# Kernel tuning notes

Measured on AMD Instinct MI355X. Metric: run time of the kernel, lower is better.

The kernel has to match this reference:

```python
import jax, jax.numpy as jnp
import numpy as np

N_NODES = 40000
N_EDGES = 640000
D_IN = 128
D_OUT = 128
ALPHA = 0.5   # real-valued complex alpha from init
Q = 0.25      # magnetic potential parameter


def setup_inputs() -> dict:
    key = jax.random.key(0)
    k = jax.random.split(key, 6)
    x = jax.random.normal(k[0], (N_NODES, D_IN), dtype=jnp.float32)
    edge_index = jax.random.randint(k[1], (2, N_EDGES), 0, N_NODES, dtype=jnp.int32)
    W1 = jax.random.normal(k[2], (D_IN, D_OUT), dtype=jnp.float32) * 0.05
    b1 = jax.random.normal(k[3], (D_OUT,), dtype=jnp.float32) * 0.05
    W2 = jax.random.normal(k[4], (D_IN, D_OUT), dtype=jnp.float32) * 0.05
    b2 = jax.random.normal(k[5], (D_OUT,), dtype=jnp.float32) * 0.05
    return {"x": x, "edge_index": edge_index, "W1": W1, "b1": b1, "W2": W2, "b2": b2}


def _magnet_spmm(x, edge_index, q):
    """y = H @ x where H = D_s^{-1/2} (A_s * exp(i*2*pi*q*(A - A^T))) D_s^{-1/2},
    A_s = 0.5*(A + A^T). Returns (y_real, y_imag); x is real (zero imag part)."""
    n = x.shape[0]
    row, col = edge_index[0], edge_index[1]
    e = row.shape[0]
    # detect whether the reverse edge (col,row) exists in the edge set
    keys = row * n + col
    rkeys = col * n + row
    sk = jnp.sort(keys)
    pos = jnp.searchsorted(sk, rkeys)
    has_rev = (pos < e) & (sk[jnp.clip(pos, 0, e - 1)] == rkeys)
    # symmetrize: each directed edge contributes 0.5 in both directions.
    # forward copy carries phase sign +1, reversed copy sign -1; phase is 0
    # when both directions exist (A - A^T = 0 there).
    r_all = jnp.concatenate([row, col])          # [2E]
    c_all = jnp.concatenate([col, row])
    sign = jnp.concatenate([jnp.ones((e,), x.dtype), -jnp.ones((e,), x.dtype)])
    hr = jnp.concatenate([has_rev, has_rev]).astype(x.dtype)
    theta = (2.0 * np.pi * q) * sign * (1.0 - hr)
    half = jnp.asarray(0.5, x.dtype)
    # symmetrized degree: deg[u] = sum_v A_s[u,v]
    deg = jax.ops.segment_sum(jnp.full((2 * e,), 0.5, x.dtype), r_all, num_segments=n)
    dinv = jnp.where(deg > 0, 1.0 / jnp.sqrt(deg), 0.0)
    scale = half * dinv[r_all] * dinv[c_all]
    val_re = scale * jnp.cos(theta)
    val_im = scale * jnp.sin(theta)
    xg = x[c_all]                                # [2E, D] gather
    y_re = jax.ops.segment_sum(val_re[:, None] * xg, r_all, num_segments=n)
    y_im = jax.ops.segment_sum(val_im[:, None] * xg, r_all, num_segments=n)
    return y_re, y_im


def reference(x, edge_index, W1, b1, W2, b2):
    y_re, y_im = _magnet_spmm(x, edge_index, Q)
    # alpha * lin1(y) + (1-alpha) * lin2(y), applied to real and imag parts
    out_re = ALPHA * (y_re @ W1 + b1) + (1.0 - ALPHA) * (y_re @ W2 + b2)
    out_im = ALPHA * (y_im @ W1 + b1) + (1.0 - ALPHA) * (y_im @ W2 + b2)
    return jnp.concatenate([out_re, out_im], axis=1)  # [N, 2*D_OUT]
```

## Files before the change

### kernel.cpp

```cpp
#include <hip/hip_runtime.h>
#include <math.h>

#define N_NODES 40000
#define D 128
#define NEDGE 640000
#define CAP 80

__device__ __forceinline__ unsigned short bf16rn(float f) {
    unsigned u = __float_as_uint(f);
    unsigned r = u + 0x7FFFu + ((u >> 16) & 1u);
    return (unsigned short)(r >> 16);
}

__global__ void init_kernel(int* __restrict__ cursorA, int* __restrict__ cursorB,
                            const float* __restrict__ W1, const float* __restrict__ b1,
                            const float* __restrict__ W2, const float* __restrict__ b2,
                            float* __restrict__ Wc, float* __restrict__ bc) {
    int i = blockIdx.x * blockDim.x + threadIdx.x;
    int stride = gridDim.x * blockDim.x;
    for (int t = i; t < N_NODES; t += stride) { cursorA[t] = 0; cursorB[t] = 0; }
    for (int t = i; t < D * D; t += stride) Wc[t] = 0.5f * (W1[t] + W2[t]);
    if (i < D) bc[i] = 0.5f * (b1[i] + b2[i]);
}

__global__ void expand_kernel(const int* __restrict__ row, const int* __restrict__ col,
                              int* __restrict__ cursorA, int* __restrict__ cursorB,
                              unsigned short* __restrict__ entries,
                              const float* __restrict__ x, unsigned short* __restrict__ xb) {
    int i = blockIdx.x * blockDim.x + threadIdx.x;
    int gstride = gridDim.x * blockDim.x;
    for (int e = i; e < NEDGE; e += gstride) {
        int r = row[e], c = col[e];
        int p1 = atomicAdd(&cursorA[r], 1);
        if (p1 < CAP) entries[(size_t)r * CAP + p1] = (unsigned short)c;
        int p2 = atomicAdd(&cursorB[c], 1);
        if (p2 < CAP) entries[(size_t)c * CAP + (CAP - 1 - p2)] = (unsigned short)r;
    }
    if (xb) {
        for (int t = i; t < N_NODES * D / 4; t += gstride) {
            float4 v = ((const float4*)x)[t];
            ushort4 o;
            o.x = bf16rn(v.x); o.y = bf16rn(v.y); o.z = bf16rn(v.z); o.w = bf16rn(v.w);
            ((ushort4*)xb)[t] = o;
        }
    }
}

template <int USE_BF16>
__global__ __launch_bounds__(256) void fused_kernel(
    const float* __restrict__ x, const unsigned short* __restrict__ xb,
    const unsigned short* __restrict__ entries,
    const int* __restrict__ cursorA, const int* __restrict__ cursorB,
    const float* __restrict__ Wc, const float* __restrict__ bc,
    float* __restrict__ out) {
    __shared__ unsigned short rawlds[4][2][CAP];
    __shared__ uint2 slds[4][2][CAP];
    __shared__ float ylds[8][260];

    int tid = threadIdx.x;
    int wave = tid >> 6, half = (tid >> 5) & 1, l = tid & 31;
    int n = wave * 2 + half;
    int u = blockIdx.x * 8 + n;

    int cA = cursorA[u], cB = cursorB[u];
    int a = min(cA, CAP);
    int b = min(cB, CAP - a);
    int m = a + b;
    int cnt = cA + cB;
    float dinv_u = (cnt > 0) ? rsqrtf(0.5f * (float)cnt) : 0.f;
    const unsigned short* eb = entries + (size_t)u * CAP;
    int gap = CAP - m;

    for (int t = l; t < m; t += 32)
        rawlds[wave][half][t] = eb[t < a ? t : t + gap];
    __builtin_amdgcn_wave_barrier();

    for (int t = l; t < m; t += 32) {
        unsigned short src = rawlds[wave][half][t];
        bool d1 = (t >= a);
        int lo = d1 ? 0 : a, hi = d1 ? a : m;
        bool rev = false;
        for (int j = lo; j < hi; ++j)
            rev |= (rawlds[wave][half][j] == src);
        int cs = cursorA[src] + cursorB[src];
        float s = 0.5f * dinv_u * rsqrtf(0.5f * (float)max(cs, 1));
        unsigned flag = 0u;
        float sval;
        if (rev) { sval = s; flag = 0x10000u; }
        else     { sval = d1 ? -s : s; }
        slds[wave][half][t] = make_uint2((unsigned)src | flag, __float_as_uint(sval));
    }
    __builtin_amdgcn_wave_barrier();

    float4 accre = make_float4(0.f, 0.f, 0.f, 0.f);
    float4 accim = make_float4(0.f, 0.f, 0.f, 0.f);

    if (USE_BF16) {
        #pragma unroll 8
        for (int i = 0; i < m; ++i) {
            uint2 t = slds[wave][half][i];
            unsigned src = t.x & 0xFFFFu;
            float s = __uint_as_float(t.y);
            bool isre = (t.x & 0x10000u) != 0u;
            float fre = isre ? s : 0.f;
            float fim = isre ? 0.f : s;
            uint2 v = ((const uint2*)(xb + (size_t)src * D))[l];
            float v0 = __uint_as_float(v.x << 16);
            float v1 = __uint_as_float(v.x & 0xFFFF0000u);
            float v2 = __uint_as_float(v.y << 16);
            float v3 = __uint_as_float(v.y & 0xFFFF0000u);
            accre.x += fre * v0; accre.y += fre * v1;
            accre.z += fre * v2; accre.w += fre * v3;
            accim.x += fim * v0; accim.y += fim * v1;
            accim.z += fim * v2; accim.w += fim * v3;
        }
    } else {
        #pragma unroll 4
        for (int i = 0; i < m; ++i) {
            uint2 t = slds[wave][half][i];
            unsigned src = t.x & 0xFFFFu;
            float s = __uint_as_float(t.y);
            bool isre = (t.x & 0x10000u) != 0u;
            float fre = isre ? s : 0.f;
            float fim = isre ? 0.f : s;
            float4 v = ((const float4*)(x + (size_t)src * D))[l];
            accre.x += fre * v.x; accre.y += fre * v.y;
            accre.z += fre * v.z; accre.w += fre * v.w;
            accim.x += fim * v.x; accim.y += fim * v.y;
            accim.z += fim * v.z; accim.w += fim * v.w;
        }
    }

    *(float4*)&ylds[n][l * 4] = accre;
    *(float4*)&ylds[n][128 + l * 4] = accim;
    __syncthreads();

    int n2 = tid >> 5, c = tid & 31;
    int u2 = blockIdx.x * 8 + n2;
    const float* yb = &ylds[n2][0];
    const float4* Wc4 = (const float4*)Wc;
    float4 ar = make_float4(0.f, 0.f, 0.f, 0.f);
    float4 ai = make_float4(0.f, 0.f, 0.f, 0.f);
    #pragma unroll 4
    for (int k = 0; k < 128; k += 4) {
        float4 yr4 = *(const float4*)&yb[k];
        float4 yi4 = *(const float4*)&yb[128 + k];
        #pragma unroll
        for (int j = 0; j < 4; ++j) {
            float4 w = Wc4[(k + j) * 32 + c];
            float yr = (j == 0) ? yr4.x : (j == 1) ? yr4.y : (j == 2) ? yr4.z : yr4.w;
            float yi = (j == 0) ? yi4.x : (j == 1) ? yi4.y : (j == 2) ? yi4.z : yi4.w;
            ar.x += yr * w.x; ar.y += yr * w.y; ar.z += yr * w.z; ar.w += yr * w.w;
            ai.x += yi * w.x; ai.y += yi * w.y; ai.z += yi * w.z; ai.w += yi * w.w;
        }
    }
    float4 bv = ((const float4*)bc)[c];
    ar.x += bv.x; ar.y += bv.y; ar.z += bv.z; ar.w += bv.w;
    ai.x += bv.x; ai.y += bv.y; ai.z += bv.z; ai.w += bv.w;
    *(float4*)&out[(size_t)u2 * 256 + c * 4] = ar;
    *(float4*)&out[(size_t)u2 * 256 + 128 + c * 4] = ai;
}

extern "C" void kernel_launch(void* const* d_in, const int* in_sizes, int n_in,
                              void* d_out, int out_size, void* d_ws, size_t ws_size,
                              hipStream_t stream) {
    const float* x  = (const float*)d_in[0];
    const int*   ei = (const int*)d_in[1];
    const float* W1 = (const float*)d_in[2];
    const float* b1 = (const float*)d_in[3];
    const float* W2 = (const float*)d_in[4];
    const float* b2 = (const float*)d_in[5];
    float* out = (float*)d_out;
    const int* row = ei;
    const int* col = ei + NEDGE;

    char* ws = (char*)d_ws;
    float*          Wc      = (float*)ws;
    float*          bc      = (float*)(ws + 65536);
    int*            cursorA = (int*)(ws + 66048);
    int*            cursorB = (int*)(ws + 226048);
    unsigned short* entries = (unsigned short*)(ws + 386048);
    const size_t xoff = 6786048;
    const size_t XBB = (size_t)N_NODES * D * 2;

    unsigned short* xb = nullptr;
    bool bf16 = false;
    if (ws_size >= xoff + XBB) {
        xb = (unsigned short*)(ws + xoff);
        bf16 = true;
    }

    init_kernel<<<512, 256, 0, stream>>>(cursorA, cursorB, W1, b1, W2, b2, Wc, bc);
    expand_kernel<<<2500, 256, 0, stream>>>(row, col, cursorA, cursorB, entries, x, xb);
    if (bf16) {
        fused_kernel<1><<<N_NODES / 8, 256, 0, stream>>>(x, xb, entries, cursorA, cursorB,
                                                         Wc, bc, out);
    } else {
        fused_kernel<0><<<N_NODES / 8, 256, 0, stream>>>(x, xb, entries, cursorA, cursorB,
                                                         Wc, bc, out);
    }
}
```

Measured before the change: 196.3 us.

## Apply combined linear layer before sparse aggregation and gather bf16 projected features

Uses linearity to reorder the computation as (H x) W = H (x W). A new dense GEMM kernel computes z = x·0.5(W1+W2) into bf16, also zeroing the cursors. The gather kernel then aggregates z directly and adds the bias, so the per-node dense projection after aggregation and its LDS staging are removed. The per-node matmul previously ran on both the real and imaginary parts, so the dense work is halved. The cost is a separate GEMM pass with an extra bf16 write and read of z, plus bf16 rounding applied after the projection instead of to x. The fp32 fallback path is dropped and a larger workspace is assumed.

```diff
diff --git a/kernel.cpp b/kernel.cpp
--- a/kernel.cpp
+++ b/kernel.cpp
@@ -5,6 +5,7 @@
 #define D 128
 #define NEDGE 640000
 #define CAP 80
+#define ZNB 64
 
 __device__ __forceinline__ unsigned short bf16rn(float f) {
     unsigned u = __float_as_uint(f);
@@ -12,21 +13,63 @@
     return (unsigned short)(r >> 16);
 }
 
-__global__ void init_kernel(int* __restrict__ cursorA, int* __restrict__ cursorB,
-                            const float* __restrict__ W1, const float* __restrict__ b1,
-                            const float* __restrict__ W2, const float* __restrict__ b2,
-                            float* __restrict__ Wc, float* __restrict__ bc) {
-    int i = blockIdx.x * blockDim.x + threadIdx.x;
-    int stride = gridDim.x * blockDim.x;
-    for (int t = i; t < N_NODES; t += stride) { cursorA[t] = 0; cursorB[t] = 0; }
-    for (int t = i; t < D * D; t += stride) Wc[t] = 0.5f * (W1[t] + W2[t]);
-    if (i < D) bc[i] = 0.5f * (b1[i] + b2[i]);
+__global__ __launch_bounds__(256) void zgemm_kernel(
+    const float* __restrict__ x, const float* __restrict__ W1, const float* __restrict__ W2,
+    unsigned short* __restrict__ z, int* __restrict__ cursorA, int* __restrict__ cursorB) {
+    int tid = threadIdx.x;
+    int gtid = blockIdx.x * 256 + tid;
+    int gstride = gridDim.x * 256;
+    for (int t = gtid; t < N_NODES; t += gstride) { cursorA[t] = 0; cursorB[t] = 0; }
+
+    __shared__ float xl[ZNB][129];
+    int node0 = blockIdx.x * ZNB;
+    const float4* xs = (const float4*)(x + (size_t)node0 * D);
+    for (int t = tid; t < ZNB * (D / 4); t += 256)
+        *(float4*)&xl[t >> 5][(t & 31) * 4] = xs[t];
+    __syncthreads();
+
+    int ng = tid >> 4;
+    int c8 = tid & 15;
+    float acc[4][8];
+    #pragma unroll
+    for (int q = 0; q < 4; ++q)
+        #pragma unroll
+        for (int j = 0; j < 8; ++j) acc[q][j] = 0.f;
+
+    const float4* W1v = (const float4*)W1;
+    const float4* W2v = (const float4*)W2;
+    #pragma unroll 2
+    for (int k = 0; k < D; ++k) {
+        float4 a1 = W1v[k * 32 + c8 * 2],     u1 = W1v[k * 32 + c8 * 2 + 1];
+        float4 a2 = W2v[k * 32 + c8 * 2],     u2 = W2v[k * 32 + c8 * 2 + 1];
+        float w[8];
+        w[0] = 0.5f * (a1.x + a2.x); w[1] = 0.5f * (a1.y + a2.y);
+        w[2] = 0.5f * (a1.z + a2.z); w[3] = 0.5f * (a1.w + a2.w);
+        w[4] = 0.5f * (u1.x + u2.x); w[5] = 0.5f * (u1.y + u2.y);
+        w[6] = 0.5f * (u1.z + u2.z); w[7] = 0.5f * (u1.w + u2.w);
+        #pragma unroll
+        for (int q = 0; q < 4; ++q) {
+            float xv = xl[ng * 4 + q][k];
+            #pragma unroll
+            for (int j = 0; j < 8; ++j) acc[q][j] += xv * w[j];
+        }
+    }
+    #pragma unroll
+    for (int q = 0; q < 4; ++q) {
+        int node = node0 + ng * 4 + q;
+        ushort4 o1, o2;
+        o1.x = bf16rn(acc[q][0]); o1.y = bf16rn(acc[q][1]);
+        o1.z = bf16rn(acc[q][2]); o1.w = bf16rn(acc[q][3]);
+        o2.x = bf16rn(acc[q][4]); o2.y = bf16rn(acc[q][5]);
+        o2.z = bf16rn(acc[q][6]); o2.w = bf16rn(acc[q][7]);
+        ushort4* zp = (ushort4*)(z + (size_t)node * D + c8 * 8);
+        zp[0] = o1; zp[1] = o2;
+    }
 }
 
 __global__ void expand_kernel(const int* __restrict__ row, const int* __restrict__ col,
                               int* __restrict__ cursorA, int* __restrict__ cursorB,
-                              unsigned short* __restrict__ entries,
-                              const float* __restrict__ x, unsigned short* __restrict__ xb) {
+                              unsigned short* __restrict__ entries) {
     int i = blockIdx.x * blockDim.x + threadIdx.x;
     int gstride = gridDim.x * blockDim.x;
     for (int e = i; e < NEDGE; e += gstride) {
@@ -36,26 +79,15 @@
         int p2 = atomicAdd(&cursorB[c], 1);
         if (p2 < CAP) entries[(size_t)c * CAP + (CAP - 1 - p2)] = (unsigned short)r;
     }
-    if (xb) {
-        for (int t = i; t < N_NODES * D / 4; t += gstride) {
-            float4 v = ((const float4*)x)[t];
-            ushort4 o;
-            o.x = bf16rn(v.x); o.y = bf16rn(v.y); o.z = bf16rn(v.z); o.w = bf16rn(v.w);
-            ((ushort4*)xb)[t] = o;
-        }
-    }
 }
 
-template <int USE_BF16>
-__global__ __launch_bounds__(256) void fused_kernel(
-    const float* __restrict__ x, const unsigned short* __restrict__ xb,
-    const unsigned short* __restrict__ entries,
+__global__ __launch_bounds__(256) void gather_kernel(
+    const unsigned short* __restrict__ z, const unsigned short* __restrict__ entries,
     const int* __restrict__ cursorA, const int* __restrict__ cursorB,
-    const float* __restrict__ Wc, const float* __restrict__ bc,
+    const float* __restrict__ b1, const float* __restrict__ b2,
     float* __restrict__ out) {
     __shared__ unsigned short rawlds[4][2][CAP];
     __shared__ uint2 slds[4][2][CAP];
-    __shared__ float ylds[8][260];
 
     int tid = threadIdx.x;
     int wave = tid >> 6, half = (tid >> 5) & 1, l = tid & 31;
@@ -95,70 +127,34 @@
     float4 accre = make_float4(0.f, 0.f, 0.f, 0.f);
     float4 accim = make_float4(0.f, 0.f, 0.f, 0.f);
 
-    if (USE_BF16) {
-        #pragma unroll 8
-        for (int i = 0; i < m; ++i) {
-            uint2 t = slds[wave][half][i];
-            unsigned src = t.x & 0xFFFFu;
-            float s = __uint_as_float(t.y);
-            bool isre = (t.x & 0x10000u) != 0u;
-            float fre = isre ? s : 0.f;
-            float fim = isre ? 0.f : s;
-            uint2 v = ((const uint2*)(xb + (size_t)src * D))[l];
-            float v0 = __uint_as_float(v.x << 16);
-            float v1 = __uint_as_float(v.x & 0xFFFF0000u);
-            float v2 = __uint_as_float(v.y << 16);
-            float v3 = __uint_as_float(v.y & 0xFFFF0000u);
-            accre.x += fre * v0; accre.y += fre * v1;
-            accre.z += fre * v2; accre.w += fre * v3;
-            accim.x += fim * v0; accim.y += fim * v1;
-            accim.z += fim * v2; accim.w += fim * v3;
-        }
-    } else {
-        #pragma unroll 4
-        for (int i = 0; i < m; ++i) {
-            uint2 t = slds[wave][half][i];
-            unsigned src = t.x & 0xFFFFu;
-            float s = __uint_as_float(t.y);
-            bool isre = (t.x & 0x10000u) != 0u;
-            float fre = isre ? s : 0.f;
-            float fim = isre ? 0.f : s;
-            float4 v = ((const float4*)(x + (size_t)src * D))[l];
-            accre.x += fre * v.x; accre.y += fre * v.y;
-            accre.z += fre * v.z; accre.w += fre * v.w;
-            accim.x += fim * v.x; accim.y += fim * v.y;
-            accim.z += fim * v.z; accim.w += fim * v.w;
-        }
+    #pragma unroll 8
+    for (int i = 0; i < m; ++i) {
+        uint2 t = slds[wave][half][i];
+        unsigned src = t.x & 0xFFFFu;
+        float s = __uint_as_float(t.y);
+        bool isre = (t.x & 0x10000u) != 0u;
+        float fre = isre ? s : 0.f;
+        float fim = isre ? 0.f : s;
+        uint2 v = ((const uint2*)(z + (size_t)src * D))[l];
+        float v0 = __uint_as_float(v.x << 16);
+        float v1 = __uint_as_float(v.x & 0xFFFF0000u);
+        float v2 = __uint_as_float(v.y << 16);
+        float v3 = __uint_as_float(v.y & 0xFFFF0000u);
+        accre.x += fre * v0; accre.y += fre * v1;
+        accre.z += fre * v2; accre.w += fre * v3;
+        accim.x += fim * v0; accim.y += fim * v1;
+        accim.z += fim * v2; accim.w += fim * v3;
     }
 
-    *(float4*)&ylds[n][l * 4] = accre;
-    *(float4*)&ylds[n][128 + l * 4] = accim;
-    __syncthreads();
+    float4 ba = ((const float4*)b1)[l];
+    float4 bb = ((const float4*)b2)[l];
+    float4 bv = make_float4(0.5f * (ba.x + bb.x), 0.5f * (ba.y + bb.y),
+                            0.5f * (ba.z + bb.z), 0.5f * (ba.w + bb.w));
+    accre.x += bv.x; accre.y += bv.y; accre.z += bv.z; accre.w += bv.w;
+    accim.x += bv.x; accim.y += bv.y; accim.z += bv.z; accim.w += bv.w;
 
-    int n2 = tid >> 5, c = tid & 31;
-    int u2 = blockIdx.x * 8 + n2;
-    const float* yb = &ylds[n2][0];
-    const float4* Wc4 = (const float4*)Wc;
-    float4 ar = make_float4(0.f, 0.f, 0.f, 0.f);
-    float4 ai = make_float4(0.f, 0.f, 0.f, 0.f);
-    #pragma unroll 4
-    for (int k = 0; k < 128; k += 4) {
-        float4 yr4 = *(const float4*)&yb[k];
-        float4 yi4 = *(const float4*)&yb[128 + k];
-        #pragma unroll
-        for (int j = 0; j < 4; ++j) {
-            float4 w = Wc4[(k + j) * 32 + c];
-            float yr = (j == 0) ? yr4.x : (j == 1) ? yr4.y : (j == 2) ? yr4.z : yr4.w;
-            float yi = (j == 0) ? yi4.x : (j == 1) ? yi4.y : (j == 2) ? yi4.z : yi4.w;
-            ar.x += yr * w.x; ar.y += yr * w.y; ar.z += yr * w.z; ar.w += yr * w.w;
-            ai.x += yi * w.x; ai.y += yi * w.y; ai.z += yi * w.z; ai.w += yi * w.w;
-        }
-    }
-    float4 bv = ((const float4*)bc)[c];
-    ar.x += bv.x; ar.y += bv.y; ar.z += bv.z; ar.w += bv.w;
-    ai.x += bv.x; ai.y += bv.y; ai.z += bv.z; ai.w += bv.w;
-    *(float4*)&out[(size_t)u2 * 256 + c * 4] = ar;
-    *(float4*)&out[(size_t)u2 * 256 + 128 + c * 4] = ai;
+    *(float4*)&out[(size_t)u * 256 + l * 4] = accre;
+    *(float4*)&out[(size_t)u * 256 + 128 + l * 4] = accim;
 }
 
 extern "C" void kernel_launch(void* const* d_in, const int* in_sizes, int n_in,
@@ -175,28 +171,12 @@
     const int* col = ei + NEDGE;
 
     char* ws = (char*)d_ws;
-    float*          Wc      = (float*)ws;
-    float*          bc      = (float*)(ws + 65536);
-    int*            cursorA = (int*)(ws + 66048);
-    int*            cursorB = (int*)(ws + 226048);
-    unsigned short* entries = (unsigned short*)(ws + 386048);
-    const size_t xoff = 6786048;
-    const size_t XBB = (size_t)N_NODES * D * 2;
+    int*            cursorA = (int*)ws;
+    int*            cursorB = (int*)(ws + 160000);
+    unsigned short* entries = (unsigned short*)(ws + 320000);
+    unsigned short* z       = (unsigned short*)(ws + 6720000);
 
-    unsigned short* xb = nullptr;
-    bool bf16 = false;
-    if (ws_size >= xoff + XBB) {
-        xb = (unsigned short*)(ws + xoff);
-        bf16 = true;
-    }
-
-    init_kernel<<<512, 256, 0, stream>>>(cursorA, cursorB, W1, b1, W2, b2, Wc, bc);
-    expand_kernel<<<2500, 256, 0, stream>>>(row, col, cursorA, cursorB, entries, x, xb);
-    if (bf16) {
-        fused_kernel<1><<<N_NODES / 8, 256, 0, stream>>>(x, xb, entries, cursorA, cursorB,
-                                                         Wc, bc, out);
-    } else {
-        fused_kernel<0><<<N_NODES / 8, 256, 0, stream>>>(x, xb, entries, cursorA, cursorB,
-                                                         Wc, bc, out);
-    }
+    zgemm_kernel<<<N_NODES / ZNB, 256, 0, stream>>>(x, W1, W2, z, cursorA, cursorB);
+    expand_kernel<<<2500, 256, 0, stream>>>(row, col, cursorA, cursorB, entries);
+    gather_kernel<<<N_NODES / 8, 256, 0, stream>>>(z, entries, cursorA, cursorB, b1, b2, out);
 }
```

Result: slower. 201.5 us (+2.7%).
